# Kernel optimization log

Hardware: AMD Instinct MI355X
Metric: run time of the kernel (lower is better)

Reference implementation:

```python
import jax, jax.numpy as jnp
import numpy as np

B, N, D = 2, 8192, 1024
H, DH = 16, 64
SEG = 512          # total_segment_len (num_longterm_mem_tokens = 0)
P = 16             # num_persist_mem_tokens
EPS = 1.1920929e-07  # torch RMSNorm eps=None -> finfo(float32).eps


def _rope(x, pos, theta=10000.0):
    # rotary-embedding-torch style: interleaved pairs, freqs repeated (n r), r=2
    d = x.shape[-1]
    inv_freq = 1.0 / (theta ** (jnp.arange(0, d, 2, dtype=jnp.float32) / d))  # [d/2]
    ang = pos[:, None] * inv_freq                                             # [n, d/2]
    cos = jnp.repeat(jnp.cos(ang), 2, axis=-1)                                # [n, d]
    sin = jnp.repeat(jnp.sin(ang), 2, axis=-1)
    x1, x2 = x[..., 0::2], x[..., 1::2]
    rot = jnp.stack((-x2, x1), axis=-1).reshape(x.shape)
    return x * cos + rot * sin


def setup_inputs() -> dict:
    key = jax.random.key(0)
    ks = jax.random.split(key, 5)
    return {
        "seq": jax.random.normal(ks[0], (B, N, D), dtype=jnp.float32),
        "w_norm": 1.0 + 0.02 * jax.random.normal(ks[1], (D,), dtype=jnp.float32),
        "Wqkv": jax.random.normal(ks[2], (D, 3 * H * DH), dtype=jnp.float32) * (D ** -0.5),
        "Wout": jax.random.normal(ks[3], (H * DH, D), dtype=jnp.float32) * ((H * DH) ** -0.5),
        "pm": 0.02 * jax.random.normal(ks[4], (2, H, P, DH), dtype=jnp.float32),
    }


def reference(seq, w_norm, Wqkv, Wout, pm):
    b, n, d = seq.shape
    w = n // SEG  # n is a multiple of SEG by construction

    # RMSNorm
    x = seq * jax.lax.rsqrt(jnp.mean(seq * seq, axis=-1, keepdims=True) + EPS) * w_norm

    # QKV projection, split heads -> [b, h, n, dh]
    qkv = x @ Wqkv
    q, k, v = jnp.split(qkv, 3, axis=-1)
    split = lambda t: t.reshape(b, n, H, DH).transpose(0, 2, 1, 3)
    q, k, v = split(q), split(k), split(v)

    # RoPE on full (global) positions before segmenting
    pos = jnp.arange(n, dtype=jnp.float32)
    q = _rope(q, pos)
    k = _rope(k, pos)

    # Segment: [b, h, n, dh] -> [b*w, h, SEG, dh]
    seg = lambda t: t.reshape(b, H, w, SEG, DH).transpose(0, 2, 1, 3, 4).reshape(b * w, H, SEG, DH)
    q, k, v = seg(q), seg(k), seg(v)

    # Prepend persistent memory KVs
    pmk = jnp.broadcast_to(pm[0], (b * w, H, P, DH))
    pmv = jnp.broadcast_to(pm[1], (b * w, H, P, DH))
    k = jnp.concatenate((pmk, k), axis=-2)  # [b*w, h, P+SEG, dh]
    v = jnp.concatenate((pmv, v), axis=-2)

    # Causal attention with kv offset P (persistent tokens always visible)
    scale = DH ** -0.5
    scores = jnp.einsum('bhid,bhjd->bhij', q, k) * scale  # [b*w, h, SEG, P+SEG]
    mask = (jnp.arange(P + SEG) - P)[None, :] <= jnp.arange(SEG)[:, None]
    scores = jnp.where(mask, scores, jnp.finfo(scores.dtype).min)
    attn = jax.nn.softmax(scores, axis=-1)
    out = jnp.einsum('bhij,bhjd->bhid', attn, v)  # [b*w, h, SEG, dh]

    # Merge heads, un-segment, output projection
    out = out.transpose(0, 2, 1, 3).reshape(b * w, SEG, H * DH)
    out = out @ Wout
    out = out.reshape(b, n, -1)
    return out
```

## Files before the change

### kernel.cpp

```cpp
#include <hip/hip_runtime.h>
#include <hip/hip_bf16.h>
#include <stdint.h>
#include <stddef.h>

typedef _Float16 f16;
typedef __attribute__((ext_vector_type(8))) _Float16 f16x8;
typedef __attribute__((ext_vector_type(4))) _Float16 f16x4;
typedef __attribute__((ext_vector_type(4))) float f32x4;
typedef __attribute__((ext_vector_type(16))) float f32x16;

#define MFMA_F16(a, b, c) __builtin_amdgcn_mfma_f32_16x16x32_f16(a, b, c, 0, 0, 0)
#define MFMA32_F16(a, b, c) __builtin_amdgcn_mfma_f32_32x32x16_f16(a, b, c, 0, 0, 0)

#define LOG2_10K_32 0.41524101186092025f

__device__ __forceinline__ uint32_t swz(uint32_t ci) {
    return (ci & ~7u) | ((ci ^ (ci >> 3)) & 7u);
}

__device__ __forceinline__ void async_ld16(void* lds, const void* g) {
    __builtin_amdgcn_global_load_lds(
        (const __attribute__((address_space(1))) void*)g,
        (__attribute__((address_space(3))) void*)lds, 16, 0, 0);
}

__global__ __launch_bounds__(256) void k_transpose_cast(
        const float* __restrict__ S, f16* __restrict__ D, int rows, int cols) {
    __shared__ float tile[32][33];
    int x = threadIdx.x & 31, y = threadIdx.x >> 5;
    int c0 = blockIdx.x * 32, r0 = blockIdx.y * 32;
#pragma unroll
    for (int i = 0; i < 32; i += 8)
        tile[y + i][x] = S[(size_t)(r0 + y + i) * cols + c0 + x];
    __syncthreads();
#pragma unroll
    for (int i = 0; i < 32; i += 8)
        D[(size_t)(c0 + y + i) * rows + r0 + x] = (f16)tile[x][y + i];
}

__global__ __launch_bounds__(256) void k_rmsnorm(
        const float* __restrict__ seq, const float* __restrict__ w, f16* __restrict__ X) {
    int row = blockIdx.x, t = threadIdx.x;
    const float4* sp = (const float4*)(seq + (size_t)row * 1024);
    float4 v = sp[t];
    float ss = v.x * v.x + v.y * v.y + v.z * v.z + v.w * v.w;
#pragma unroll
    for (int off = 32; off >= 1; off >>= 1) ss += __shfl_xor(ss, off, 64);
    __shared__ float red[4];
    if ((t & 63) == 0) red[t >> 6] = ss;
    __syncthreads();
    float tot = red[0] + red[1] + red[2] + red[3];
    float rs = rsqrtf(tot * (1.0f / 1024.0f) + 1.1920929e-07f);
    const float4* wp = (const float4*)w;
    float4 wv = wp[t];
    f16x4 o;
    o[0] = (f16)(v.x * rs * wv.x);
    o[1] = (f16)(v.y * rs * wv.y);
    o[2] = (f16)(v.z * rs * wv.z);
    o[3] = (f16)(v.w * rs * wv.w);
    *(f16x4*)(X + (size_t)row * 1024 + t * 4) = o;
}

__global__ __launch_bounds__(256) void k_gemm_qkv(
        const f16* __restrict__ A, const f16* __restrict__ BT,
        f16* __restrict__ Qb, f16* __restrict__ Kb, f16* __restrict__ Vt) {
    const int K = 1024;
    __shared__ f16 As[128 * 32];
    __shared__ f16 Bs[128 * 32];
    const int t = threadIdx.x;
    const int lane = t & 63, wave = t >> 6, l32 = lane & 31, half = lane >> 5;
    const int m0 = blockIdx.y * 128, n0 = blockIdx.x * 128;
    const int wm = (wave & 1) * 64, wn = (wave >> 1) * 64;
    f32x16 acc[2][2];
#pragma unroll
    for (int i = 0; i < 2; i++)
#pragma unroll
        for (int j = 0; j < 2; j++)
#pragma unroll
            for (int r = 0; r < 16; r++) acc[i][j][r] = 0.f;

    uint32_t aoff[2][2], boff[2][2];
#pragma unroll
    for (int bk = 0; bk < 2; bk++)
#pragma unroll
        for (int ks = 0; ks < 2; ks++) {
            aoff[bk][ks] = swz((uint32_t)(wm + bk * 32 + l32) * 4 + ks * 2 + half) * 16;
            boff[bk][ks] = swz((uint32_t)(wn + bk * 32 + l32) * 4 + ks * 2 + half) * 16;
        }
    uint32_t c0 = swz(t), c1 = swz(t + 256);
    const f16* Ag0 = A + (size_t)(m0 + (c0 >> 2)) * K + (c0 & 3) * 8;
    const f16* Ag1 = A + (size_t)(m0 + (c1 >> 2)) * K + (c1 & 3) * 8;
    const f16* Bg0 = BT + (size_t)(n0 + (c0 >> 2)) * K + (c0 & 3) * 8;
    const f16* Bg1 = BT + (size_t)(n0 + (c1 >> 2)) * K + (c1 & 3) * 8;
    char* AsB = (char*)As;
    char* BsB = (char*)Bs;

    for (int k0 = 0; k0 < K; k0 += 32) {
        __syncthreads();
        async_ld16(AsB + t * 16, Ag0 + k0);
        async_ld16(AsB + (t + 256) * 16, Ag1 + k0);
        async_ld16(BsB + t * 16, Bg0 + k0);
        async_ld16(BsB + (t + 256) * 16, Bg1 + k0);
        __builtin_amdgcn_s_waitcnt(0x0f70);
        __syncthreads();
        f16x8 a[2][2], b[2][2];
#pragma unroll
        for (int bk = 0; bk < 2; bk++)
#pragma unroll
            for (int ks = 0; ks < 2; ks++) {
                a[bk][ks] = *(const f16x8*)(AsB + aoff[bk][ks]);
                b[bk][ks] = *(const f16x8*)(BsB + boff[bk][ks]);
            }
#pragma unroll
        for (int mb = 0; mb < 2; mb++)
#pragma unroll
            for (int nb = 0; nb < 2; nb++) {
                acc[mb][nb] = MFMA32_F16(b[nb][0], a[mb][0], acc[mb][nb]);
                acc[mb][nb] = MFMA32_F16(b[nb][1], a[mb][1], acc[mb][nb]);
            }
    }

    const int region = n0 >> 10;
#pragma unroll
    for (int mb = 0; mb < 2; mb++) {
        int row = m0 + wm + mb * 32 + l32;
        int b_ = row >> 13, n_ = row & 8191;
        int win = n_ >> 9, i_ = n_ & 511;
        float fn = (float)n_;
#pragma unroll
        for (int nb = 0; nb < 2; nb++) {
            int colb = n0 + wn + nb * 32 + half * 4;
            int cr = colb & 1023;
            int h = cr >> 6;
            int d0 = cr & 63;
            int wh = ((b_ * 16 + win) << 4) + h;
            if (region < 2) {
                f16* base = (region == 0)
                    ? (Qb + ((size_t)wh * 512 + i_) * 64)
                    : (Kb + ((size_t)wh * 576 + 16 + i_) * 64);
#pragma unroll
                for (int q = 0; q < 4; q++) {
                    int d = d0 + q * 8;
                    float j0f = (float)(d >> 1);
                    float ang0 = fn * exp2f(-LOG2_10K_32 * j0f);
                    float ang1 = fn * exp2f(-LOG2_10K_32 * (j0f + 1.0f));
                    float s0, c0f, s1, c1f;
                    sincosf(ang0, &s0, &c0f);
                    sincosf(ang1, &s1, &c1f);
                    float x0 = (float)(f16)acc[mb][nb][q * 4 + 0];
                    float x1 = (float)(f16)acc[mb][nb][q * 4 + 1];
                    float x2 = (float)(f16)acc[mb][nb][q * 4 + 2];
                    float x3 = (float)(f16)acc[mb][nb][q * 4 + 3];
                    f16x4 ov;
                    ov[0] = (f16)(x0 * c0f - x1 * s0);
                    ov[1] = (f16)(x1 * c0f + x0 * s0);
                    ov[2] = (f16)(x2 * c1f - x3 * s1);
                    ov[3] = (f16)(x3 * c1f + x2 * s1);
                    *(f16x4*)(base + d) = ov;
                }
            } else {
                f16* vbase = Vt + (size_t)wh * 36864 + 16 + i_;
#pragma unroll
                for (int q = 0; q < 4; q++)
#pragma unroll
                    for (int r = 0; r < 4; r++)
                        vbase[(size_t)(d0 + q * 8 + r) * 576] = (f16)acc[mb][nb][q * 4 + r];
            }
        }
    }
}

__global__ __launch_bounds__(256) void k_gemm_out(
        const f16* __restrict__ A, const f16* __restrict__ BT,
        float* __restrict__ C, int M, int N, int K) {
    __shared__ f16 As[128 * 32];
    __shared__ f16 Bs[128 * 32];
    const int t = threadIdx.x;
    const int lane = t & 63, wave = t >> 6, l32 = lane & 31, half = lane >> 5;
    const int m0 = blockIdx.y * 128, n0 = blockIdx.x * 128;
    const int wm = (wave & 1) * 64, wn = (wave >> 1) * 64;
    f32x16 acc[2][2];
#pragma unroll
    for (int i = 0; i < 2; i++)
#pragma unroll
        for (int j = 0; j < 2; j++)
#pragma unroll
            for (int r = 0; r < 16; r++) acc[i][j][r] = 0.f;

    uint32_t aoff[2][2], boff[2][2];
#pragma unroll
    for (int bk = 0; bk < 2; bk++)
#pragma unroll
        for (int ks = 0; ks < 2; ks++) {
            aoff[bk][ks] = swz((uint32_t)(wm + bk * 32 + l32) * 4 + ks * 2 + half) * 16;
            boff[bk][ks] = swz((uint32_t)(wn + bk * 32 + l32) * 4 + ks * 2 + half) * 16;
        }
    uint32_t c0 = swz(t), c1 = swz(t + 256);
    const f16* Ag0 = A + (size_t)(m0 + (c0 >> 2)) * K + (c0 & 3) * 8;
    const f16* Ag1 = A + (size_t)(m0 + (c1 >> 2)) * K + (c1 & 3) * 8;
    const f16* Bg0 = BT + (size_t)(n0 + (c0 >> 2)) * K + (c0 & 3) * 8;
    const f16* Bg1 = BT + (size_t)(n0 + (c1 >> 2)) * K + (c1 & 3) * 8;
    char* AsB = (char*)As;
    char* BsB = (char*)Bs;

    for (int k0 = 0; k0 < K; k0 += 32) {
        __syncthreads();
        async_ld16(AsB + t * 16, Ag0 + k0);
        async_ld16(AsB + (t + 256) * 16, Ag1 + k0);
        async_ld16(BsB + t * 16, Bg0 + k0);
        async_ld16(BsB + (t + 256) * 16, Bg1 + k0);
        __builtin_amdgcn_s_waitcnt(0x0f70);
        __syncthreads();
        f16x8 a[2][2], b[2][2];
#pragma unroll
        for (int bk = 0; bk < 2; bk++)
#pragma unroll
            for (int ks = 0; ks < 2; ks++) {
                a[bk][ks] = *(const f16x8*)(AsB + aoff[bk][ks]);
                b[bk][ks] = *(const f16x8*)(BsB + boff[bk][ks]);
            }
#pragma unroll
        for (int mb = 0; mb < 2; mb++)
#pragma unroll
            for (int nb = 0; nb < 2; nb++) {
                acc[mb][nb] = MFMA32_F16(b[nb][0], a[mb][0], acc[mb][nb]);
                acc[mb][nb] = MFMA32_F16(b[nb][1], a[mb][1], acc[mb][nb]);
            }
    }
#pragma unroll
    for (int mb = 0; mb < 2; mb++) {
        int row = m0 + wm + mb * 32 + l32;
#pragma unroll
        for (int nb = 0; nb < 2; nb++) {
            int colb = n0 + wn + nb * 32 + half * 4;
#pragma unroll
            for (int q = 0; q < 4; q++) {
                f32x4 ov;
#pragma unroll
                for (int r = 0; r < 4; r++) ov[r] = acc[mb][nb][q * 4 + r];
                *(f32x4*)(C + (size_t)row * N + colb + q * 8) = ov;
            }
        }
    }
}

__global__ __launch_bounds__(256) void k_pmpad(
        const float* __restrict__ pm, f16* __restrict__ Kb, f16* __restrict__ Vt) {
    int wh = blockIdx.x, h = wh & 15, t = threadIdx.x;
    const float* pk = pm + (size_t)h * 1024;
    f16* kb = Kb + (size_t)wh * 36864;
    int e0 = t * 4;
#pragma unroll
    for (int k = 0; k < 4; k++) kb[e0 + k] = (f16)pk[e0 + k];
#pragma unroll
    for (int k = 0; k < 12; k++) kb[33792 + t + k * 256] = (f16)0.f;
    const float* pv = pm + 16384 + (size_t)h * 1024;
    f16* vb = Vt + (size_t)wh * 36864;
    {
        int d = t & 63, s4 = (t >> 6) * 4;
#pragma unroll
        for (int k = 0; k < 4; k++)
            vb[(size_t)d * 576 + s4 + k] = (f16)pv[(s4 + k) * 64 + d];
    }
    {
        int d = t >> 2, rep = t & 3;
#pragma unroll
        for (int m = 0; m < 12; m++)
            vb[(size_t)d * 576 + 528 + rep * 12 + m] = (f16)0.f;
    }
}

__global__ __launch_bounds__(256) void k_attn(
        const f16* __restrict__ Q, const f16* __restrict__ Kb,
        const f16* __restrict__ Vt, f16* __restrict__ AO) {
    const int qt = blockIdx.x, wh = blockIdx.y;
    const int i0 = qt * 64;
    const int t = threadIdx.x, lane = t & 63, wave = t >> 6, quad = lane >> 4, l16 = lane & 15;
    __shared__ f16 Ks[64 * 64];
    __shared__ f16 Vs[64 * 64];
    __shared__ f16 Ps[4][16][80];

    const int ig = i0 + wave * 16 + l16;
    const f16* qptr = Q + ((size_t)wh * 512 + ig) * 64 + quad * 8;
    f16x8 qf0 = *(const f16x8*)(qptr);
    f16x8 qf1 = *(const f16x8*)(qptr + 32);

    const f32x4 zero = {0.f, 0.f, 0.f, 0.f};
    f32x4 o[4];
#pragma unroll
    for (int i = 0; i < 4; i++) o[i] = zero;
    float m_l = -1e30f, l_l = 0.f;

    uint32_t c0 = swz(t), c1 = swz(t + 256);
    const f16* kg0 = Kb + ((size_t)wh * 576 + (c0 >> 3)) * 64 + (c0 & 7) * 8;
    const f16* kg1 = Kb + ((size_t)wh * 576 + (c1 >> 3)) * 64 + (c1 & 7) * 8;
    const f16* vg0 = Vt + ((size_t)wh * 64 + (c0 >> 3)) * 576 + (c0 & 7) * 8;
    const f16* vg1 = Vt + ((size_t)wh * 64 + (c1 >> 3)) * 576 + (c1 & 7) * 8;
    char* KsB = (char*)Ks;
    char* VsB = (char*)Vs;

    uint32_t boff[4][2];
#pragma unroll
    for (int i = 0; i < 4; i++)
#pragma unroll
        for (int f = 0; f < 2; f++)
            boff[i][f] = swz((uint32_t)(i * 16 + l16) * 8 + f * 4 + quad) * 16;

    f16* psrow = &Ps[wave][l16][0];
    const int njt = (qt + 2 < 9) ? (qt + 2) : 9;

    for (int jt = 0; jt < njt; jt++) {
        const int j0 = jt * 64;
        __syncthreads();
        async_ld16(KsB + t * 16, kg0 + (size_t)j0 * 64);
        async_ld16(KsB + (t + 256) * 16, kg1 + (size_t)j0 * 64);
        async_ld16(VsB + t * 16, vg0 + j0);
        async_ld16(VsB + (t + 256) * 16, vg1 + j0);
        __builtin_amdgcn_s_waitcnt(0x0f70);
        __syncthreads();

        f32x4 s[4];
#pragma unroll
        for (int jb = 0; jb < 4; jb++) {
            f16x8 kv0 = *(const f16x8*)(KsB + boff[jb][0]);
            f16x8 kv1 = *(const f16x8*)(KsB + boff[jb][1]);
            f32x4 z = zero;
            z = MFMA_F16(kv0, qf0, z);
            z = MFMA_F16(kv1, qf1, z);
            s[jb] = z;
        }
        float mx = -1e30f;
#pragma unroll
        for (int jb = 0; jb < 4; jb++)
#pragma unroll
            for (int r = 0; r < 4; r++) {
                int jg = j0 + jb * 16 + quad * 4 + r;
                bool ok = (jg <= ig + 16) && (jg < 528);
                float val = ok ? s[jb][r] * 0.125f : -1e30f;
                s[jb][r] = val;
                mx = fmaxf(mx, val);
            }
        mx = fmaxf(mx, __shfl_xor(mx, 16, 64));
        mx = fmaxf(mx, __shfl_xor(mx, 32, 64));
        float mnew = fmaxf(m_l, mx);
        float alpha = __expf(m_l - mnew);
        m_l = mnew;
        float rsum = 0.f;
#pragma unroll
        for (int jb = 0; jb < 4; jb++) {
            f16x4 pw;
#pragma unroll
            for (int r = 0; r < 4; r++) {
                float p = __expf(s[jb][r] - mnew);
                rsum += p;
                pw[r] = (f16)p;
            }
            *(f16x4*)(psrow + jb * 16 + quad * 4) = pw;
        }
        rsum += __shfl_xor(rsum, 16, 64);
        rsum += __shfl_xor(rsum, 32, 64);
        l_l = l_l * alpha + rsum;
#pragma unroll
        for (int nd = 0; nd < 4; nd++) o[nd] *= alpha;
        __syncthreads();

        f16x8 pb0 = *(const f16x8*)(psrow + quad * 8);
        f16x8 pb1 = *(const f16x8*)(psrow + 32 + quad * 8);
#pragma unroll
        for (int nd = 0; nd < 4; nd++) {
            f16x8 v0 = *(const f16x8*)(VsB + boff[nd][0]);
            f16x8 v1 = *(const f16x8*)(VsB + boff[nd][1]);
            o[nd] = MFMA_F16(v0, pb0, o[nd]);
            o[nd] = MFMA_F16(v1, pb1, o[nd]);
        }
    }

    const int bw = wh >> 4, h = wh & 15;
    float inv = 1.f / l_l;
    f16* dst = AO + ((size_t)bw * 512 + ig) * 1024 + h * 64 + quad * 4;
#pragma unroll
    for (int nd = 0; nd < 4; nd++) {
        f16x4 ov;
#pragma unroll
        for (int r = 0; r < 4; r++) ov[r] = (f16)(o[nd][r] * inv);
        *(f16x4*)(dst + nd * 16) = ov;
    }
}

extern "C" void kernel_launch(void* const* d_in, const int* in_sizes, int n_in,
                              void* d_out, int out_size, void* d_ws, size_t ws_size,
                              hipStream_t stream) {
    const float* seq   = (const float*)d_in[0];
    const float* wnorm = (const float*)d_in[1];
    const float* Wqkv  = (const float*)d_in[2];
    const float* Wout  = (const float*)d_in[3];
    const float* pm    = (const float*)d_in[4];
    float* out = (float*)d_out;
    char* ws = (char*)d_ws;

    f16* WqkvT = (f16*)(ws + 0);
    f16* WoutT = (f16*)(ws + 6291456);
    f16* X     = (f16*)(ws + 8388608);
    f16* Qb    = (f16*)(ws + 41943040);
    f16* AO    = (f16*)(ws + 75497472);
    f16* Kb    = (f16*)(ws + 109051904);
    f16* Vt    = (f16*)(ws + 146800640);

    k_transpose_cast<<<dim3(96, 32), 256, 0, stream>>>(Wqkv, WqkvT, 1024, 3072);
    k_transpose_cast<<<dim3(32, 32), 256, 0, stream>>>(Wout, WoutT, 1024, 1024);
    k_rmsnorm<<<16384, 256, 0, stream>>>(seq, wnorm, X);
    k_pmpad<<<512, 256, 0, stream>>>(pm, Kb, Vt);
    k_gemm_qkv<<<dim3(24, 128), 256, 0, stream>>>(X, WqkvT, Qb, Kb, Vt);
    k_attn<<<dim3(8, 512), 256, 0, stream>>>(Qb, Kb, Vt, AO);
    k_gemm_out<<<dim3(8, 128), 256, 0, stream>>>(AO, WoutT, out, 16384, 1024, 1024);
}
```

Before: 432.7 us.

## Rework QKV and output GEMMs with 256x256 tiles and 4-stage async LDS pipeline

Both projection GEMMs move from 128x128 tiles with 256 threads and a single-buffered load-wait-compute loop to 256x256 tiles with 512 threads. Operands are staged through a 4-deep ring of LDS buffers filled by async global-to-LDS loads issued three k-steps ahead. A and B prefetches are interleaved with MFMA phases that run at raised wave priority. The aim is to hide global load latency and raise operand reuse per byte loaded. In exchange each block uses 128KB of static LDS, which limits occupancy to one block per CU, and the output GEMM grid shrinks to 256 blocks.

After: 500.4 us. 15.6% more time.

```diff
diff --git a/kernel.cpp b/kernel.cpp
--- a/kernel.cpp
+++ b/kernel.cpp
@@ -61,68 +61,116 @@
     *(f16x4*)(X + (size_t)row * 1024 + t * 4) = o;
 }
 
-__global__ __launch_bounds__(256) void k_gemm_qkv(
+__global__ __launch_bounds__(512, 2) void k_gemm_qkv(
         const f16* __restrict__ A, const f16* __restrict__ BT,
         f16* __restrict__ Qb, f16* __restrict__ Kb, f16* __restrict__ Vt) {
     const int K = 1024;
-    __shared__ f16 As[128 * 32];
-    __shared__ f16 Bs[128 * 32];
+    const int NT = 32;
+    __shared__ __align__(16) char ldsA[65536];
+    __shared__ __align__(16) char ldsB[65536];
     const int t = threadIdx.x;
     const int lane = t & 63, wave = t >> 6, l32 = lane & 31, half = lane >> 5;
-    const int m0 = blockIdx.y * 128, n0 = blockIdx.x * 128;
-    const int wm = (wave & 1) * 64, wn = (wave >> 1) * 64;
-    f32x16 acc[2][2];
-#pragma unroll
-    for (int i = 0; i < 2; i++)
+    const int m0 = blockIdx.y * 256, n0 = blockIdx.x * 256;
+    const int wm = (wave >> 2) * 128, wn = (wave & 3) * 64;
+
+    f32x16 acc[4][2];
+#pragma unroll
+    for (int i = 0; i < 4; i++)
 #pragma unroll
         for (int j = 0; j < 2; j++)
 #pragma unroll
             for (int r = 0; r < 16; r++) acc[i][j][r] = 0.f;
 
-    uint32_t aoff[2][2], boff[2][2];
-#pragma unroll
-    for (int bk = 0; bk < 2; bk++)
-#pragma unroll
-        for (int ks = 0; ks < 2; ks++) {
-            aoff[bk][ks] = swz((uint32_t)(wm + bk * 32 + l32) * 4 + ks * 2 + half) * 16;
-            boff[bk][ks] = swz((uint32_t)(wn + bk * 32 + l32) * 4 + ks * 2 + half) * 16;
-        }
-    uint32_t c0 = swz(t), c1 = swz(t + 256);
-    const f16* Ag0 = A + (size_t)(m0 + (c0 >> 2)) * K + (c0 & 3) * 8;
-    const f16* Ag1 = A + (size_t)(m0 + (c1 >> 2)) * K + (c1 & 3) * 8;
-    const f16* Bg0 = BT + (size_t)(n0 + (c0 >> 2)) * K + (c0 & 3) * 8;
-    const f16* Bg1 = BT + (size_t)(n0 + (c1 >> 2)) * K + (c1 & 3) * 8;
-    char* AsB = (char*)As;
-    char* BsB = (char*)Bs;
-
-    for (int k0 = 0; k0 < K; k0 += 32) {
-        __syncthreads();
-        async_ld16(AsB + t * 16, Ag0 + k0);
-        async_ld16(AsB + (t + 256) * 16, Ag1 + k0);
-        async_ld16(BsB + t * 16, Bg0 + k0);
-        async_ld16(BsB + (t + 256) * 16, Bg1 + k0);
-        __builtin_amdgcn_s_waitcnt(0x0f70);
-        __syncthreads();
-        f16x8 a[2][2], b[2][2];
-#pragma unroll
-        for (int bk = 0; bk < 2; bk++)
-#pragma unroll
-            for (int ks = 0; ks < 2; ks++) {
-                a[bk][ks] = *(const f16x8*)(AsB + aoff[bk][ks]);
-                b[bk][ks] = *(const f16x8*)(BsB + boff[bk][ks]);
-            }
-#pragma unroll
-        for (int mb = 0; mb < 2; mb++)
-#pragma unroll
-            for (int nb = 0; nb < 2; nb++) {
-                acc[mb][nb] = MFMA32_F16(b[nb][0], a[mb][0], acc[mb][nb]);
-                acc[mb][nb] = MFMA32_F16(b[nb][1], a[mb][1], acc[mb][nb]);
-            }
+    uint32_t aoff[4][2], boff[2][2];
+#pragma unroll
+    for (int mb = 0; mb < 4; mb++)
+#pragma unroll
+        for (int ks = 0; ks < 2; ks++)
+            aoff[mb][ks] = swz((uint32_t)(wm + mb * 32 + l32) * 4 + ks * 2 + half) * 16;
+#pragma unroll
+    for (int nb = 0; nb < 2; nb++)
+#pragma unroll
+        for (int ks = 0; ks < 2; ks++)
+            boff[nb][ks] = swz((uint32_t)(wn + nb * 32 + l32) * 4 + ks * 2 + half) * 16;
+
+    uint32_t g0 = swz((uint32_t)t), g1 = swz((uint32_t)t + 512);
+    const f16* Ag0 = A + (size_t)(m0 + (g0 >> 2)) * K + (g0 & 3) * 8;
+    const f16* Ag1 = A + (size_t)(m0 + (g1 >> 2)) * K + (g1 & 3) * 8;
+    const f16* Bg0 = BT + (size_t)(n0 + (g0 >> 2)) * K + (g0 & 3) * 8;
+    const f16* Bg1 = BT + (size_t)(n0 + (g1 >> 2)) * K + (g1 & 3) * 8;
+
+#pragma unroll
+    for (int p = 0; p < 3; ++p) {
+        char* dA = ldsA + p * 16384;
+        async_ld16(dA + t * 16, Ag0 + p * 32);
+        async_ld16(dA + (t + 512) * 16, Ag1 + p * 32);
+        char* dB = ldsB + p * 16384;
+        async_ld16(dB + t * 16, Bg0 + p * 32);
+        async_ld16(dB + (t + 512) * 16, Bg1 + p * 32);
+    }
+    __builtin_amdgcn_s_waitcnt(0x0f78);
+    __builtin_amdgcn_s_barrier();
+    __builtin_amdgcn_sched_barrier(0);
+
+#pragma unroll 4
+    for (int kt = 0; kt < NT; ++kt) {
+        char* As_s = ldsA + (kt & 3) * 16384;
+        char* Bs_s = ldsB + (kt & 3) * 16384;
+        f16x8 a00 = *(const f16x8*)(As_s + aoff[0][0]);
+        f16x8 a01 = *(const f16x8*)(As_s + aoff[0][1]);
+        f16x8 a10 = *(const f16x8*)(As_s + aoff[1][0]);
+        f16x8 a11 = *(const f16x8*)(As_s + aoff[1][1]);
+        f16x8 b00 = *(const f16x8*)(Bs_s + boff[0][0]);
+        f16x8 b01 = *(const f16x8*)(Bs_s + boff[0][1]);
+        f16x8 b10 = *(const f16x8*)(Bs_s + boff[1][0]);
+        f16x8 b11 = *(const f16x8*)(Bs_s + boff[1][1]);
+        if (kt < NT - 3) {
+            char* dA = ldsA + ((kt + 3) & 3) * 16384;
+            async_ld16(dA + t * 16, Ag0 + (kt + 3) * 32);
+            async_ld16(dA + (t + 512) * 16, Ag1 + (kt + 3) * 32);
+        }
+        __builtin_amdgcn_s_barrier();
+        __builtin_amdgcn_s_setprio(1);
+        acc[0][0] = MFMA32_F16(b00, a00, acc[0][0]);
+        acc[0][0] = MFMA32_F16(b01, a01, acc[0][0]);
+        acc[0][1] = MFMA32_F16(b10, a00, acc[0][1]);
+        acc[0][1] = MFMA32_F16(b11, a01, acc[0][1]);
+        acc[1][0] = MFMA32_F16(b00, a10, acc[1][0]);
+        acc[1][0] = MFMA32_F16(b01, a11, acc[1][0]);
+        acc[1][1] = MFMA32_F16(b10, a10, acc[1][1]);
+        acc[1][1] = MFMA32_F16(b11, a11, acc[1][1]);
+        __builtin_amdgcn_s_setprio(0);
+        __builtin_amdgcn_s_barrier();
+        f16x8 a20 = *(const f16x8*)(As_s + aoff[2][0]);
+        f16x8 a21 = *(const f16x8*)(As_s + aoff[2][1]);
+        f16x8 a30 = *(const f16x8*)(As_s + aoff[3][0]);
+        f16x8 a31 = *(const f16x8*)(As_s + aoff[3][1]);
+        if (kt < NT - 3) {
+            char* dB = ldsB + ((kt + 3) & 3) * 16384;
+            async_ld16(dB + t * 16, Bg0 + (kt + 3) * 32);
+            async_ld16(dB + (t + 512) * 16, Bg1 + (kt + 3) * 32);
+        }
+        __builtin_amdgcn_s_barrier();
+        __builtin_amdgcn_s_setprio(1);
+        acc[2][0] = MFMA32_F16(b00, a20, acc[2][0]);
+        acc[2][0] = MFMA32_F16(b01, a21, acc[2][0]);
+        acc[2][1] = MFMA32_F16(b10, a20, acc[2][1]);
+        acc[2][1] = MFMA32_F16(b11, a21, acc[2][1]);
+        acc[3][0] = MFMA32_F16(b00, a30, acc[3][0]);
+        acc[3][0] = MFMA32_F16(b01, a31, acc[3][0]);
+        acc[3][1] = MFMA32_F16(b10, a30, acc[3][1]);
+        acc[3][1] = MFMA32_F16(b11, a31, acc[3][1]);
+        __builtin_amdgcn_s_setprio(0);
+        if (kt < NT - 3)       __builtin_amdgcn_s_waitcnt(0x0f78);
+        else if (kt == NT - 3) __builtin_amdgcn_s_waitcnt(0x0f74);
+        else if (kt == NT - 2) __builtin_amdgcn_s_waitcnt(0x0f70);
+        __builtin_amdgcn_s_barrier();
+        __builtin_amdgcn_sched_barrier(0);
     }
 
     const int region = n0 >> 10;
 #pragma unroll
-    for (int mb = 0; mb < 2; mb++) {
+    for (int mb = 0; mb < 4; mb++) {
         int row = m0 + wm + mb * 32 + l32;
         int b_ = row >> 13, n_ = row & 8191;
         int win = n_ >> 9, i_ = n_ & 511;
@@ -170,65 +218,115 @@
     }
 }
 
-__global__ __launch_bounds__(256) void k_gemm_out(
+__global__ __launch_bounds__(512, 2) void k_gemm_out(
         const f16* __restrict__ A, const f16* __restrict__ BT,
-        float* __restrict__ C, int M, int N, int K) {
-    __shared__ f16 As[128 * 32];
-    __shared__ f16 Bs[128 * 32];
+        float* __restrict__ C, int M, int N, int Kp) {
+    const int K = 1024;
+    const int NT = 32;
+    __shared__ __align__(16) char ldsA[65536];
+    __shared__ __align__(16) char ldsB[65536];
     const int t = threadIdx.x;
     const int lane = t & 63, wave = t >> 6, l32 = lane & 31, half = lane >> 5;
-    const int m0 = blockIdx.y * 128, n0 = blockIdx.x * 128;
-    const int wm = (wave & 1) * 64, wn = (wave >> 1) * 64;
-    f32x16 acc[2][2];
-#pragma unroll
-    for (int i = 0; i < 2; i++)
+    const int m0 = blockIdx.y * 256, n0 = blockIdx.x * 256;
+    const int wm = (wave >> 2) * 128, wn = (wave & 3) * 64;
+
+    f32x16 acc[4][2];
+#pragma unroll
+    for (int i = 0; i < 4; i++)
 #pragma unroll
         for (int j = 0; j < 2; j++)
 #pragma unroll
             for (int r = 0; r < 16; r++) acc[i][j][r] = 0.f;
 
-    uint32_t aoff[2][2], boff[2][2];
-#pragma unroll
-    for (int bk = 0; bk < 2; bk++)
-#pragma unroll
-        for (int ks = 0; ks < 2; ks++) {
-            aoff[bk][ks] = swz((uint32_t)(wm + bk * 32 + l32) * 4 + ks * 2 + half) * 16;
-            boff[bk][ks] = swz((uint32_t)(wn + bk * 32 + l32) * 4 + ks * 2 + half) * 16;
-        }
-    uint32_t c0 = swz(t), c1 = swz(t + 256);
-    const f16* Ag0 = A + (size_t)(m0 + (c0 >> 2)) * K + (c0 & 3) * 8;
-    const f16* Ag1 = A + (size_t)(m0 + (c1 >> 2)) * K + (c1 & 3) * 8;
-    const f16* Bg0 = BT + (size_t)(n0 + (c0 >> 2)) * K + (c0 & 3) * 8;
-    const f16* Bg1 = BT + (size_t)(n0 + (c1 >> 2)) * K + (c1 & 3) * 8;
-    char* AsB = (char*)As;
-    char* BsB = (char*)Bs;
-
-    for (int k0 = 0; k0 < K; k0 += 32) {
-        __syncthreads();
-        async_ld16(AsB + t * 16, Ag0 + k0);
-        async_ld16(AsB + (t + 256) * 16, Ag1 + k0);
-        async_ld16(BsB + t * 16, Bg0 + k0);
-        async_ld16(BsB + (t + 256) * 16, Bg1 + k0);
-        __builtin_amdgcn_s_waitcnt(0x0f70);
-        __syncthreads();
-        f16x8 a[2][2], b[2][2];
-#pragma unroll
-        for (int bk = 0; bk < 2; bk++)
-#pragma unroll
-            for (int ks = 0; ks < 2; ks++) {
-                a[bk][ks] = *(const f16x8*)(AsB + aoff[bk][ks]);
-                b[bk][ks] = *(const f16x8*)(BsB + boff[bk][ks]);
-            }
-#pragma unroll
-        for (int mb = 0; mb < 2; mb++)
-#pragma unroll
-            for (int nb = 0; nb < 2; nb++) {
-                acc[mb][nb] = MFMA32_F16(b[nb][0], a[mb][0], acc[mb][nb]);
-                acc[mb][nb] = MFMA32_F16(b[nb][1], a[mb][1], acc[mb][nb]);
-            }
-    }
-#pragma unroll
-    for (int mb = 0; mb < 2; mb++) {
+    uint32_t aoff[4][2], boff[2][2];
+#pragma unroll
+    for (int mb = 0; mb < 4; mb++)
+#pragma unroll
+        for (int ks = 0; ks < 2; ks++)
+            aoff[mb][ks] = swz((uint32_t)(wm + mb * 32 + l32) * 4 + ks * 2 + half) * 16;
+#pragma unroll
+    for (int nb = 0; nb < 2; nb++)
+#pragma unroll
+        for (int ks = 0; ks < 2; ks++)
+            boff[nb][ks] = swz((uint32_t)(wn + nb * 32 + l32) * 4 + ks * 2 + half) * 16;
+
+    uint32_t g0 = swz((uint32_t)t), g1 = swz((uint32_t)t + 512);
+    const f16* Ag0 = A + (size_t)(m0 + (g0 >> 2)) * K + (g0 & 3) * 8;
+    const f16* Ag1 = A + (size_t)(m0 + (g1 >> 2)) * K + (g1 & 3) * 8;
+    const f16* Bg0 = BT + (size_t)(n0 + (g0 >> 2)) * K + (g0 & 3) * 8;
+    const f16* Bg1 = BT + (size_t)(n0 + (g1 >> 2)) * K + (g1 & 3) * 8;
+
+#pragma unroll
+    for (int p = 0; p < 3; ++p) {
+        char* dA = ldsA + p * 16384;
+        async_ld16(dA + t * 16, Ag0 + p * 32);
+        async_ld16(dA + (t + 512) * 16, Ag1 + p * 32);
+        char* dB = ldsB + p * 16384;
+        async_ld16(dB + t * 16, Bg0 + p * 32);
+        async_ld16(dB + (t + 512) * 16, Bg1 + p * 32);
+    }
+    __builtin_amdgcn_s_waitcnt(0x0f78);
+    __builtin_amdgcn_s_barrier();
+    __builtin_amdgcn_sched_barrier(0);
+
+#pragma unroll 4
+    for (int kt = 0; kt < NT; ++kt) {
+        char* As_s = ldsA + (kt & 3) * 16384;
+        char* Bs_s = ldsB + (kt & 3) * 16384;
+        f16x8 a00 = *(const f16x8*)(As_s + aoff[0][0]);
+        f16x8 a01 = *(const f16x8*)(As_s + aoff[0][1]);
+        f16x8 a10 = *(const f16x8*)(As_s + aoff[1][0]);
+        f16x8 a11 = *(const f16x8*)(As_s + aoff[1][1]);
+        f16x8 b00 = *(const f16x8*)(Bs_s + boff[0][0]);
+        f16x8 b01 = *(const f16x8*)(Bs_s + boff[0][1]);
+        f16x8 b10 = *(const f16x8*)(Bs_s + boff[1][0]);
+        f16x8 b11 = *(const f16x8*)(Bs_s + boff[1][1]);
+        if (kt < NT - 3) {
+            char* dA = ldsA + ((kt + 3) & 3) * 16384;
+            async_ld16(dA + t * 16, Ag0 + (kt + 3) * 32);
+            async_ld16(dA + (t + 512) * 16, Ag1 + (kt + 3) * 32);
+        }
+        __builtin_amdgcn_s_barrier();
+        __builtin_amdgcn_s_setprio(1);
+        acc[0][0] = MFMA32_F16(b00, a00, acc[0][0]);
+        acc[0][0] = MFMA32_F16(b01, a01, acc[0][0]);
+        acc[0][1] = MFMA32_F16(b10, a00, acc[0][1]);
+        acc[0][1] = MFMA32_F16(b11, a01, acc[0][1]);
+        acc[1][0] = MFMA32_F16(b00, a10, acc[1][0]);
+        acc[1][0] = MFMA32_F16(b01, a11, acc[1][0]);
+        acc[1][1] = MFMA32_F16(b10, a10, acc[1][1]);
+        acc[1][1] = MFMA32_F16(b11, a11, acc[1][1]);
+        __builtin_amdgcn_s_setprio(0);
+        __builtin_amdgcn_s_barrier();
+        f16x8 a20 = *(const f16x8*)(As_s + aoff[2][0]);
+        f16x8 a21 = *(const f16x8*)(As_s + aoff[2][1]);
+        f16x8 a30 = *(const f16x8*)(As_s + aoff[3][0]);
+        f16x8 a31 = *(const f16x8*)(As_s + aoff[3][1]);
+        if (kt < NT - 3) {
+            char* dB = ldsB + ((kt + 3) & 3) * 16384;
+            async_ld16(dB + t * 16, Bg0 + (kt + 3) * 32);
+            async_ld16(dB + (t + 512) * 16, Bg1 + (kt + 3) * 32);
+        }
+        __builtin_amdgcn_s_barrier();
+        __builtin_amdgcn_s_setprio(1);
+        acc[2][0] = MFMA32_F16(b00, a20, acc[2][0]);
+        acc[2][0] = MFMA32_F16(b01, a21, acc[2][0]);
+        acc[2][1] = MFMA32_F16(b10, a20, acc[2][1]);
+        acc[2][1] = MFMA32_F16(b11, a21, acc[2][1]);
+        acc[3][0] = MFMA32_F16(b00, a30, acc[3][0]);
+        acc[3][0] = MFMA32_F16(b01, a31, acc[3][0]);
+        acc[3][1] = MFMA32_F16(b10, a30, acc[3][1]);
+        acc[3][1] = MFMA32_F16(b11, a31, acc[3][1]);
+        __builtin_amdgcn_s_setprio(0);
+        if (kt < NT - 3)       __builtin_amdgcn_s_waitcnt(0x0f78);
+        else if (kt == NT - 3) __builtin_amdgcn_s_waitcnt(0x0f74);
+        else if (kt == NT - 2) __builtin_amdgcn_s_waitcnt(0x0f70);
+        __builtin_amdgcn_s_barrier();
+        __builtin_amdgcn_sched_barrier(0);
+    }
+
+#pragma unroll
+    for (int mb = 0; mb < 4; mb++) {
         int row = m0 + wm + mb * 32 + l32;
 #pragma unroll
         for (int nb = 0; nb < 2; nb++) {
@@ -242,6 +340,7 @@
             }
         }
     }
+    (void)M; (void)Kp;
 }
 
 __global__ __launch_bounds__(256) void k_pmpad(
@@ -410,7 +509,7 @@
     k_transpose_cast<<<dim3(32, 32), 256, 0, stream>>>(Wout, WoutT, 1024, 1024);
     k_rmsnorm<<<16384, 256, 0, stream>>>(seq, wnorm, X);
     k_pmpad<<<512, 256, 0, stream>>>(pm, Kb, Vt);
-    k_gemm_qkv<<<dim3(24, 128), 256, 0, stream>>>(X, WqkvT, Qb, Kb, Vt);
+    k_gemm_qkv<<<dim3(12, 64), 512, 0, stream>>>(X, WqkvT, Qb, Kb, Vt);
     k_attn<<<dim3(8, 512), 256, 0, stream>>>(Qb, Kb, Vt, AO);
-    k_gemm_out<<<dim3(8, 128), 256, 0, stream>>>(AO, WoutT, out, 16384, 1024, 1024);
-}
+    k_gemm_out<<<dim3(4, 64), 512, 0, stream>>>(AO, WoutT, out, 16384, 1024, 1024);
+}
```

## Multi-stage async LDS pipeline for QKV and output GEMMs

Applied to the files above, without the earlier changes.

Both GEMM kernels now use a 4-slot LDS ring buffer with three K-tiles prefetched via async global-to-LDS loads, so global loads overlap the MFMA work and each iteration needs one barrier instead of two. Wave priority is raised around the MFMA block, and launch bounds request two blocks per CU. The cost is 64KB of LDS per block, which limits occupancy, plus careful vmcnt waits at the tail of the loop. The output GEMM now hardcodes K=1024 and ignores the K argument.

After: 430.9 us. Within noise of the previous version (-0.4%).

```diff
diff --git a/kernel.cpp b/kernel.cpp
--- a/kernel.cpp
+++ b/kernel.cpp
@@ -61,12 +61,13 @@
     *(f16x4*)(X + (size_t)row * 1024 + t * 4) = o;
 }
 
-__global__ __launch_bounds__(256) void k_gemm_qkv(
+__global__ __launch_bounds__(256, 2) void k_gemm_qkv(
         const f16* __restrict__ A, const f16* __restrict__ BT,
         f16* __restrict__ Qb, f16* __restrict__ Kb, f16* __restrict__ Vt) {
     const int K = 1024;
-    __shared__ f16 As[128 * 32];
-    __shared__ f16 Bs[128 * 32];
+    const int NT = 32;
+    __shared__ __align__(16) char AsB[4 * 8192];
+    __shared__ __align__(16) char BsB[4 * 8192];
     const int t = threadIdx.x;
     const int lane = t & 63, wave = t >> 6, l32 = lane & 31, half = lane >> 5;
     const int m0 = blockIdx.y * 128, n0 = blockIdx.x * 128;
@@ -92,25 +93,41 @@
     const f16* Ag1 = A + (size_t)(m0 + (c1 >> 2)) * K + (c1 & 3) * 8;
     const f16* Bg0 = BT + (size_t)(n0 + (c0 >> 2)) * K + (c0 & 3) * 8;
     const f16* Bg1 = BT + (size_t)(n0 + (c1 >> 2)) * K + (c1 & 3) * 8;
-    char* AsB = (char*)As;
-    char* BsB = (char*)Bs;
-
-    for (int k0 = 0; k0 < K; k0 += 32) {
-        __syncthreads();
-        async_ld16(AsB + t * 16, Ag0 + k0);
-        async_ld16(AsB + (t + 256) * 16, Ag1 + k0);
-        async_ld16(BsB + t * 16, Bg0 + k0);
-        async_ld16(BsB + (t + 256) * 16, Bg1 + k0);
-        __builtin_amdgcn_s_waitcnt(0x0f70);
-        __syncthreads();
+
+#pragma unroll
+    for (int p = 0; p < 3; ++p) {
+        char* dA = AsB + p * 8192;
+        char* dB = BsB + p * 8192;
+        async_ld16(dA + t * 16, Ag0 + p * 32);
+        async_ld16(dA + (t + 256) * 16, Ag1 + p * 32);
+        async_ld16(dB + t * 16, Bg0 + p * 32);
+        async_ld16(dB + (t + 256) * 16, Bg1 + p * 32);
+    }
+    __builtin_amdgcn_s_waitcnt(0x0f78);
+    __builtin_amdgcn_s_barrier();
+    __builtin_amdgcn_sched_barrier(0);
+
+#pragma unroll 4
+    for (int kt = 0; kt < NT; ++kt) {
+        char* As_s = AsB + (kt & 3) * 8192;
+        char* Bs_s = BsB + (kt & 3) * 8192;
         f16x8 a[2][2], b[2][2];
 #pragma unroll
         for (int bk = 0; bk < 2; bk++)
 #pragma unroll
             for (int ks = 0; ks < 2; ks++) {
-                a[bk][ks] = *(const f16x8*)(AsB + aoff[bk][ks]);
-                b[bk][ks] = *(const f16x8*)(BsB + boff[bk][ks]);
-            }
+                a[bk][ks] = *(const f16x8*)(As_s + aoff[bk][ks]);
+                b[bk][ks] = *(const f16x8*)(Bs_s + boff[bk][ks]);
+            }
+        if (kt < NT - 3) {
+            char* dA = AsB + ((kt + 3) & 3) * 8192;
+            char* dB = BsB + ((kt + 3) & 3) * 8192;
+            async_ld16(dA + t * 16, Ag0 + (kt + 3) * 32);
+            async_ld16(dA + (t + 256) * 16, Ag1 + (kt + 3) * 32);
+            async_ld16(dB + t * 16, Bg0 + (kt + 3) * 32);
+            async_ld16(dB + (t + 256) * 16, Bg1 + (kt + 3) * 32);
+        }
+        __builtin_amdgcn_s_setprio(1);
 #pragma unroll
         for (int mb = 0; mb < 2; mb++)
 #pragma unroll
@@ -118,6 +135,12 @@
                 acc[mb][nb] = MFMA32_F16(b[nb][0], a[mb][0], acc[mb][nb]);
                 acc[mb][nb] = MFMA32_F16(b[nb][1], a[mb][1], acc[mb][nb]);
             }
+        __builtin_amdgcn_s_setprio(0);
+        if (kt < NT - 3)       __builtin_amdgcn_s_waitcnt(0x0f78);
+        else if (kt == NT - 3) __builtin_amdgcn_s_waitcnt(0x0f74);
+        else if (kt == NT - 2) __builtin_amdgcn_s_waitcnt(0x0f70);
+        __builtin_amdgcn_s_barrier();
+        __builtin_amdgcn_sched_barrier(0);
     }
 
     const int region = n0 >> 10;
@@ -170,11 +193,13 @@
     }
 }
 
-__global__ __launch_bounds__(256) void k_gemm_out(
+__global__ __launch_bounds__(256, 2) void k_gemm_out(
         const f16* __restrict__ A, const f16* __restrict__ BT,
-        float* __restrict__ C, int M, int N, int K) {
-    __shared__ f16 As[128 * 32];
-    __shared__ f16 Bs[128 * 32];
+        float* __restrict__ C, int M, int N, int Kp) {
+    const int K = 1024;
+    const int NT = 32;
+    __shared__ __align__(16) char AsB[4 * 8192];
+    __shared__ __align__(16) char BsB[4 * 8192];
     const int t = threadIdx.x;
     const int lane = t & 63, wave = t >> 6, l32 = lane & 31, half = lane >> 5;
     const int m0 = blockIdx.y * 128, n0 = blockIdx.x * 128;
@@ -200,25 +225,41 @@
     const f16* Ag1 = A + (size_t)(m0 + (c1 >> 2)) * K + (c1 & 3) * 8;
     const f16* Bg0 = BT + (size_t)(n0 + (c0 >> 2)) * K + (c0 & 3) * 8;
     const f16* Bg1 = BT + (size_t)(n0 + (c1 >> 2)) * K + (c1 & 3) * 8;
-    char* AsB = (char*)As;
-    char* BsB = (char*)Bs;
-
-    for (int k0 = 0; k0 < K; k0 += 32) {
-        __syncthreads();
-        async_ld16(AsB + t * 16, Ag0 + k0);
-        async_ld16(AsB + (t + 256) * 16, Ag1 + k0);
-        async_ld16(BsB + t * 16, Bg0 + k0);
-        async_ld16(BsB + (t + 256) * 16, Bg1 + k0);
-        __builtin_amdgcn_s_waitcnt(0x0f70);
-        __syncthreads();
+
+#pragma unroll
+    for (int p = 0; p < 3; ++p) {
+        char* dA = AsB + p * 8192;
+        char* dB = BsB + p * 8192;
+        async_ld16(dA + t * 16, Ag0 + p * 32);
+        async_ld16(dA + (t + 256) * 16, Ag1 + p * 32);
+        async_ld16(dB + t * 16, Bg0 + p * 32);
+        async_ld16(dB + (t + 256) * 16, Bg1 + p * 32);
+    }
+    __builtin_amdgcn_s_waitcnt(0x0f78);
+    __builtin_amdgcn_s_barrier();
+    __builtin_amdgcn_sched_barrier(0);
+
+#pragma unroll 4
+    for (int kt = 0; kt < NT; ++kt) {
+        char* As_s = AsB + (kt & 3) * 8192;
+        char* Bs_s = BsB + (kt & 3) * 8192;
         f16x8 a[2][2], b[2][2];
 #pragma unroll
         for (int bk = 0; bk < 2; bk++)
 #pragma unroll
             for (int ks = 0; ks < 2; ks++) {
-                a[bk][ks] = *(const f16x8*)(AsB + aoff[bk][ks]);
-                b[bk][ks] = *(const f16x8*)(BsB + boff[bk][ks]);
-            }
+                a[bk][ks] = *(const f16x8*)(As_s + aoff[bk][ks]);
+                b[bk][ks] = *(const f16x8*)(Bs_s + boff[bk][ks]);
+            }
+        if (kt < NT - 3) {
+            char* dA = AsB + ((kt + 3) & 3) * 8192;
+            char* dB = BsB + ((kt + 3) & 3) * 8192;
+            async_ld16(dA + t * 16, Ag0 + (kt + 3) * 32);
+            async_ld16(dA + (t + 256) * 16, Ag1 + (kt + 3) * 32);
+            async_ld16(dB + t * 16, Bg0 + (kt + 3) * 32);
+            async_ld16(dB + (t + 256) * 16, Bg1 + (kt + 3) * 32);
+        }
+        __builtin_amdgcn_s_setprio(1);
 #pragma unroll
         for (int mb = 0; mb < 2; mb++)
 #pragma unroll
@@ -226,7 +267,14 @@
                 acc[mb][nb] = MFMA32_F16(b[nb][0], a[mb][0], acc[mb][nb]);
                 acc[mb][nb] = MFMA32_F16(b[nb][1], a[mb][1], acc[mb][nb]);
             }
-    }
+        __builtin_amdgcn_s_setprio(0);
+        if (kt < NT - 3)       __builtin_amdgcn_s_waitcnt(0x0f78);
+        else if (kt == NT - 3) __builtin_amdgcn_s_waitcnt(0x0f74);
+        else if (kt == NT - 2) __builtin_amdgcn_s_waitcnt(0x0f70);
+        __builtin_amdgcn_s_barrier();
+        __builtin_amdgcn_sched_barrier(0);
+    }
+
 #pragma unroll
     for (int mb = 0; mb < 2; mb++) {
         int row = m0 + wm + mb * 32 + l32;
@@ -242,6 +290,7 @@
             }
         }
     }
+    (void)M; (void)Kp;
 }
 
 __global__ __launch_bounds__(256) void k_pmpad(
```

## Double-buffer K/V tiles in attention kernel to overlap loads with compute

Applied to the files above, without the earlier changes.

Splits the K and V shared-memory tiles into two buffers and prefetches the next key tile while the current one is being computed. The block-wide barrier before reading the P tile becomes a per-wave LDS waitcnt plus a sched_barrier, which relies on each wave reading only its own P rows. This leaves one barrier per iteration instead of three and is meant to hide global-to-LDS latency. The cost is doubled LDS for K and V, which could lower occupancy.

Measured after the change: 454.2 us. 4.9% more time.

```diff
diff --git a/kernel.cpp b/kernel.cpp
--- a/kernel.cpp
+++ b/kernel.cpp
@@ -276,8 +276,8 @@
     const int qt = blockIdx.x, wh = blockIdx.y;
     const int i0 = qt * 64;
     const int t = threadIdx.x, lane = t & 63, wave = t >> 6, quad = lane >> 4, l16 = lane & 15;
-    __shared__ f16 Ks[64 * 64];
-    __shared__ f16 Vs[64 * 64];
+    __shared__ f16 Ks[2][64 * 64];
+    __shared__ f16 Vs[2][64 * 64];
     __shared__ f16 Ps[4][16][80];
 
     const int ig = i0 + wave * 16 + l16;
@@ -309,21 +309,30 @@
     f16* psrow = &Ps[wave][l16][0];
     const int njt = (qt + 2 < 9) ? (qt + 2) : 9;
 
+    async_ld16(KsB + t * 16, kg0);
+    async_ld16(KsB + (t + 256) * 16, kg1);
+    async_ld16(VsB + t * 16, vg0);
+    async_ld16(VsB + (t + 256) * 16, vg1);
+    __builtin_amdgcn_s_waitcnt(0x0f70);
+    __syncthreads();
+
     for (int jt = 0; jt < njt; jt++) {
         const int j0 = jt * 64;
-        __syncthreads();
-        async_ld16(KsB + t * 16, kg0 + (size_t)j0 * 64);
-        async_ld16(KsB + (t + 256) * 16, kg1 + (size_t)j0 * 64);
-        async_ld16(VsB + t * 16, vg0 + j0);
-        async_ld16(VsB + (t + 256) * 16, vg1 + j0);
-        __builtin_amdgcn_s_waitcnt(0x0f70);
-        __syncthreads();
+        const uint32_t cb = (uint32_t)(jt & 1) * 8192;
+        if (jt + 1 < njt) {
+            const uint32_t pb_ = 8192 - cb;
+            const size_t j1 = (size_t)(j0 + 64);
+            async_ld16(KsB + pb_ + t * 16, kg0 + j1 * 64);
+            async_ld16(KsB + pb_ + (t + 256) * 16, kg1 + j1 * 64);
+            async_ld16(VsB + pb_ + t * 16, vg0 + j1);
+            async_ld16(VsB + pb_ + (t + 256) * 16, vg1 + j1);
+        }
 
         f32x4 s[4];
 #pragma unroll
         for (int jb = 0; jb < 4; jb++) {
-            f16x8 kv0 = *(const f16x8*)(KsB + boff[jb][0]);
-            f16x8 kv1 = *(const f16x8*)(KsB + boff[jb][1]);
+            f16x8 kv0 = *(const f16x8*)(KsB + cb + boff[jb][0]);
+            f16x8 kv1 = *(const f16x8*)(KsB + cb + boff[jb][1]);
             f32x4 z = zero;
             z = MFMA_F16(kv0, qf0, z);
             z = MFMA_F16(kv1, qf1, z);
@@ -362,17 +371,22 @@
         l_l = l_l * alpha + rsum;
 #pragma unroll
         for (int nd = 0; nd < 4; nd++) o[nd] *= alpha;
-        __syncthreads();
+
+        __builtin_amdgcn_s_waitcnt(0xc07f);
+        __builtin_amdgcn_sched_barrier(0);
 
         f16x8 pb0 = *(const f16x8*)(psrow + quad * 8);
         f16x8 pb1 = *(const f16x8*)(psrow + 32 + quad * 8);
 #pragma unroll
         for (int nd = 0; nd < 4; nd++) {
-            f16x8 v0 = *(const f16x8*)(VsB + boff[nd][0]);
-            f16x8 v1 = *(const f16x8*)(VsB + boff[nd][1]);
+            f16x8 v0 = *(const f16x8*)(VsB + cb + boff[nd][0]);
+            f16x8 v1 = *(const f16x8*)(VsB + cb + boff[nd][1]);
             o[nd] = MFMA_F16(v0, pb0, o[nd]);
             o[nd] = MFMA_F16(v1, pb1, o[nd]);
         }
+
+        __builtin_amdgcn_s_waitcnt(0x0f70);
+        __syncthreads();
     }
 
     const int bw = wh >> 4, h = wh & 15;
```
